# Kernel tuning notes

Hardware: AMD Instinct MI355X
Metric: run time of the kernel (lower is better)

## Reference

```python
import jax, jax.numpy as jnp
import numpy as np
import math

B, T, D = 4, 4096, 512
K_CACHE = 16

def _layernorm(x, g, b, eps=1e-5):
    mu = x.mean(-1, keepdims=True)
    var = ((x - mu) ** 2).mean(-1, keepdims=True)
    return (x - mu) / jnp.sqrt(var + eps) * g + b

def _shift1(x):
    # prepend zero along time axis, drop last: x_prev[t] = x[t-1]
    return jnp.pad(x, ((0, 0), (1, 0), (0, 0)))[:, :-1]

def mipt_parallel_scan(p, theta, inp_re, inp_im):
    # Faithful replication of the torch loop: ceil(log2(T+1)) iterations,
    # each combining with the element shifted by ONE position (as written).
    Bt, Tt, Dt = p.shape
    a_re = (1.0 - p) * jnp.cos(theta)
    a_im = (1.0 - p) * jnp.sin(theta)
    b_re, b_im = inp_re, inp_im
    mask = (jnp.arange(Tt) >= 1)[None, :, None]
    steps = math.ceil(math.log2(Tt + 1))
    for _ in range(steps):
        ar_p, ai_p = _shift1(a_re), _shift1(a_im)
        br_p, bi_p = _shift1(b_re), _shift1(b_im)
        new_a_re = a_re * ar_p - a_im * ai_p
        new_a_im = a_re * ai_p + a_im * ar_p
        new_b_re = a_re * br_p - a_im * bi_p + b_re
        new_b_im = a_re * bi_p + a_im * br_p + b_im
        a_re = jnp.where(mask, new_a_re, a_re)
        a_im = jnp.where(mask, new_a_im, a_im)
        b_re = jnp.where(mask, new_b_re, b_re)
        b_im = jnp.where(mask, new_b_im, b_im)
    return b_re, b_im

def setup_inputs() -> dict:
    key = jax.random.key(0)
    ks = jax.random.split(key, 32)
    s = 0.02
    def W(k, i, o):
        return jax.random.normal(k, (i, o), jnp.float32) * s
    inp = {
        'x': jax.random.normal(ks[0], (B, T, D), jnp.float32),
        'ln1_g': jnp.ones((D,), jnp.float32), 'ln1_b': jnp.zeros((D,), jnp.float32),
        'ln2_g': jnp.ones((D,), jnp.float32), 'ln2_b': jnp.zeros((D,), jnp.float32),
        'Wp_w': W(ks[1], D, D), 'Wp_b': jnp.zeros((D,), jnp.float32),
        'Wt_w': W(ks[2], D, D), 'Wt_b': jnp.zeros((D,), jnp.float32),
        'Wr_w': W(ks[3], D, D), 'Wr_b': jnp.zeros((D,), jnp.float32),
        'Wi_w': W(ks[4], D, D), 'Wi_b': jnp.zeros((D,), jnp.float32),
        'Wk_w': W(ks[5], D, D), 'Wk_b': jnp.zeros((D,), jnp.float32),
        'Wv_w': W(ks[6], D, D), 'Wv_b': jnp.zeros((D,), jnp.float32),
        'Wq_w': W(ks[7], D, D), 'Wq_b': jnp.zeros((D,), jnp.float32),
        'gate_w': W(ks[8], D, 1), 'gate_b': jnp.zeros((1,), jnp.float32),
        'ffn1_w': W(ks[9], D, 4 * D), 'ffn1_b': jnp.zeros((4 * D,), jnp.float32),
        'ffn2_w': W(ks[10], 4 * D, D), 'ffn2_b': jnp.zeros((D,), jnp.float32),
    }
    return inp

def reference(x, ln1_g, ln1_b, ln2_g, ln2_b, Wp_w, Wp_b, Wt_w, Wt_b, Wr_w, Wr_b,
              Wi_w, Wi_b, Wk_w, Wk_b, Wv_w, Wv_b, Wq_w, Wq_b, gate_w, gate_b,
              ffn1_w, ffn1_b, ffn2_w, ffn2_b):
    Bx, Tx, Dx = x.shape
    residual = x
    xn = _layernorm(x, ln1_g, ln1_b)
    p = jax.nn.sigmoid(xn @ Wp_w + Wp_b)
    theta = xn @ Wt_w + Wt_b
    inp_re = xn @ Wr_w + Wr_b
    inp_im = xn @ Wi_w + Wi_b
    h_re, _h_im = mipt_parallel_scan(p, theta, inp_re, inp_im)
    h_mean = h_re.mean(axis=1)  # [B, D]
    # CausalSparseCache (eval mode)
    p_scalar = p.mean(axis=-1)  # [B, T]
    K = min(K_CACHE, Tx)
    _, topk_idx = jax.lax.top_k(p_scalar, K)  # [B, K]
    idx = jnp.broadcast_to(topk_idx[:, :, None], (Bx, K, Dx))
    h_topk = jnp.take_along_axis(h_re, idx, axis=1)  # [B, K, D]
    keys = h_topk @ Wk_w + Wk_b
    values = h_topk @ Wv_w + Wv_b
    query = (h_mean @ Wq_w + Wq_b)[:, None, :]  # [B, 1, D]
    scores = jnp.einsum('bqd,bkd->bqk', query, keys) / math.sqrt(Dx)
    attn = jax.nn.softmax(scores, axis=-1)
    cache_out = jnp.einsum('bqk,bkd->bqd', attn, values)[:, 0]  # [B, D]
    g = jax.nn.sigmoid(h_mean @ gate_w + gate_b)  # [B, 1]
    out = h_mean + g * cache_out
    h = h_re + residual
    hn = _layernorm(h, ln2_g, ln2_b)
    ffn = jax.nn.gelu(hn @ ffn1_w + ffn1_b, approximate=False) @ ffn2_w + ffn2_b
    h = h + ffn
    return (h, out)
```

## Files before the change

kernel.cpp:

```cpp
#include <hip/hip_runtime.h>
#include <hip/hip_bf16.h>
#include <cstdint>
#include <cstddef>

typedef __bf16 bf16;
typedef __attribute__((ext_vector_type(8))) __bf16 bf16x8;
typedef __attribute__((ext_vector_type(4))) __bf16 bf16x4;
typedef __attribute__((ext_vector_type(4))) float f32x4;

#define BB 4
#define TT 4096
#define DD 512
#define MM (BB * TT)
#define OUT1_OFF ((size_t)MM * DD)

typedef __attribute__((address_space(1))) void as1_void;
typedef __attribute__((address_space(3))) void as3_void;

__device__ __forceinline__ void gl_lds16(const void* g, void* l) {
    __builtin_amdgcn_global_load_lds((as1_void*)(uintptr_t)g,
                                     (as3_void*)(uintptr_t)l, 16, 0, 0);
}

#define SIGM(x) (__builtin_amdgcn_rcpf(1.f + __expf(-(x))))

__global__ void transpose_bf16(const float* __restrict__ in, bf16* __restrict__ out,
                               int R, int C) {
    __shared__ float tile[32][33];
    const int c0 = blockIdx.x * 32, r0 = blockIdx.y * 32;
    const int tx = threadIdx.x, ty = threadIdx.y;
#pragma unroll
    for (int i = 0; i < 32; i += 8)
        tile[ty + i][tx] = in[(size_t)(r0 + ty + i) * C + (c0 + tx)];
    __syncthreads();
#pragma unroll
    for (int i = 0; i < 32; i += 8)
        out[(size_t)(c0 + ty + i) * R + (r0 + tx)] = (bf16)tile[tx][ty + i];
}

__global__ void pack_bias(const float* __restrict__ a, const float* __restrict__ b,
                          const float* __restrict__ c, const float* __restrict__ d,
                          float* __restrict__ o) {
    const int i = blockIdx.x * 256 + threadIdx.x;
    if (i < 2048) {
        const float* s = (i < 512) ? a : (i < 1024) ? b : (i < 1536) ? c : d;
        o[i] = s[i & 511];
    }
}

__global__ void zero_kernel(float* __restrict__ p, int n) {
    const int i = blockIdx.x * 256 + threadIdx.x;
    if (i < n) p[i] = 0.f;
}

__global__ __launch_bounds__(256) void ln_kernel(
    const float* __restrict__ X, const bf16* __restrict__ Xadd,
    const float* __restrict__ gw, const float* __restrict__ bw,
    bf16* __restrict__ out) {
    const int row = blockIdx.x * 4 + (threadIdx.x >> 6);
    const int lane = threadIdx.x & 63;
    const float* xr = X + (size_t)row * DD + lane * 8;
    float v[8];
    float4 v0 = *(const float4*)xr;
    float4 v1 = *(const float4*)(xr + 4);
    v[0] = v0.x; v[1] = v0.y; v[2] = v0.z; v[3] = v0.w;
    v[4] = v1.x; v[5] = v1.y; v[6] = v1.z; v[7] = v1.w;
    if (Xadd) {
        const bf16x8 a8 = *(const bf16x8*)(Xadd + (size_t)row * DD + lane * 8);
#pragma unroll
        for (int i = 0; i < 8; ++i) v[i] += (float)a8[i];
    }
    float s = 0.f, ss = 0.f;
#pragma unroll
    for (int i = 0; i < 8; ++i) { s += v[i]; ss += v[i] * v[i]; }
#pragma unroll
    for (int o = 32; o; o >>= 1) { s += __shfl_down(s, o); ss += __shfl_down(ss, o); }
    s = __shfl(s, 0); ss = __shfl(ss, 0);
    const float mu = s * (1.f / DD);
    const float var = ss * (1.f / DD) - mu * mu;
    const float rstd = rsqrtf(var + 1e-5f);
    bf16x8 o8;
#pragma unroll
    for (int i = 0; i < 8; ++i)
        o8[i] = (bf16)((v[i] - mu) * rstd * gw[lane * 8 + i] + bw[lane * 8 + i]);
    *(bf16x8*)(out + (size_t)row * DD + lane * 8) = o8;
}

#define MF(a_, b_, c_) c_ = __builtin_amdgcn_mfma_f32_16x16x32_bf16(a_, b_, c_, 0, 0, 0)

template <int MODE>
__global__ __launch_bounds__(256) void gemm_bt(
    const bf16* __restrict__ A, const bf16* __restrict__ Bt,
    const float* __restrict__ bias, void* __restrict__ Cout,
    void* __restrict__ Cout2,
    const bf16* __restrict__ add1, const float* __restrict__ add2,
    int M, int N, int K) {
    __shared__ bf16 As[3][4096];
    __shared__ bf16 Bs[3][4096];
    const int tid = threadIdx.x;
    const int lane = tid & 63;
    const int wv = tid >> 6;
    const int wr = wv >> 1, wc = wv & 1;
    const int nb = N >> 7;
    const int nwg = gridDim.x;
    int bx = blockIdx.x;
    if ((nwg & 7) == 0) bx = (bx & 7) * (nwg >> 3) + (bx >> 3);
    const int bm = bx / nb, bn = bx % nb;
    const int m0 = bm << 7, n0 = bn << 7;

    const int srow = tid >> 2;
    const int scol = (((tid & 3) ^ ((tid >> 3) & 3)) << 3);
    const bf16* Asrc = A + (size_t)(m0 + srow) * K + scol;
    const bf16* Bsrc = Bt + (size_t)(n0 + srow) * K + scol;
    const size_t rstep = (size_t)64 * K;

    const int lr = lane & 15, lg = lane >> 4;
    const int sel = ((lg ^ ((lr >> 1) & 3)) << 3);
    const int aoff = (wr * 64 + lr) * 32 + sel;
    const int boff = (wc * 64 + lr) * 32 + sel;

#define STG(buf, k0)                                                \
    do {                                                            \
        gl_lds16(Asrc + (k0),         &As[buf][wv * 512]);          \
        gl_lds16(Asrc + (k0) + rstep, &As[buf][wv * 512 + 2048]);   \
        gl_lds16(Bsrc + (k0),         &Bs[buf][wv * 512]);          \
        gl_lds16(Bsrc + (k0) + rstep, &Bs[buf][wv * 512 + 2048]);   \
    } while (0)

    f32x4 acc00 = {}, acc01 = {}, acc02 = {}, acc03 = {};
    f32x4 acc10 = {}, acc11 = {}, acc12 = {}, acc13 = {};
    f32x4 acc20 = {}, acc21 = {}, acc22 = {}, acc23 = {};
    f32x4 acc30 = {}, acc31 = {}, acc32 = {}, acc33 = {};

    const int NT = K >> 5;
    STG(0, 0);
    STG(1, 32);
    int cur = 0;
    for (int t = 0; t < NT; ++t) {
        if (t + 1 < NT) asm volatile("s_waitcnt vmcnt(4)" ::: "memory");
        else            asm volatile("s_waitcnt vmcnt(0)" ::: "memory");
        __builtin_amdgcn_s_barrier();
        asm volatile("" ::: "memory");
        const bf16* Ab = As[cur];
        const bf16* Bb = Bs[cur];
        bf16x8 af0 = *(const bf16x8*)&Ab[aoff];
        bf16x8 af1 = *(const bf16x8*)&Ab[aoff + 512];
        bf16x8 af2 = *(const bf16x8*)&Ab[aoff + 1024];
        bf16x8 af3 = *(const bf16x8*)&Ab[aoff + 1536];
        bf16x8 bf0 = *(const bf16x8*)&Bb[boff];
        bf16x8 bf1 = *(const bf16x8*)&Bb[boff + 512];
        bf16x8 bf2 = *(const bf16x8*)&Bb[boff + 1024];
        bf16x8 bf3 = *(const bf16x8*)&Bb[boff + 1536];
        if (t + 2 < NT) {
            const int stg = (cur == 0) ? 2 : cur - 1;
            STG(stg, (t + 2) << 5);
        }
        MF(af0, bf0, acc00); MF(af0, bf1, acc01); MF(af0, bf2, acc02); MF(af0, bf3, acc03);
        MF(af1, bf0, acc10); MF(af1, bf1, acc11); MF(af1, bf2, acc12); MF(af1, bf3, acc13);
        MF(af2, bf0, acc20); MF(af2, bf1, acc21); MF(af2, bf2, acc22); MF(af2, bf3, acc23);
        MF(af3, bf0, acc30); MF(af3, bf1, acc31); MF(af3, bf2, acc32); MF(af3, bf3, acc33);
        cur = (cur == 2) ? 0 : cur + 1;
    }
#undef STG

    if constexpr (MODE == 0) {
        const int cls = n0 >> 9;
        if (cls == 0) {
            const int pidx = (n0 + wc * 64) >> 6;
#define EPI0(mi, A0, A1, A2, A3)                                              \
    do {                                                                      \
        const int gmb = m0 + wr * 64 + mi * 16 + 4 * lg;                      \
        const int dbase = n0 + wc * 64 + lr;                                  \
        const float b0_ = bias[dbase], b1_ = bias[dbase + 16],                \
                    b2_ = bias[dbase + 32], b3_ = bias[dbase + 48];           \
        _Pragma("unroll")                                                     \
        for (int i = 0; i < 4; ++i) {                                         \
            const int row = gmb + i;                                          \
            const float p0 = SIGM(A0[i] + b0_);                               \
            const float p1 = SIGM(A1[i] + b1_);                               \
            const float p2 = SIGM(A2[i] + b2_);                               \
            const float p3 = SIGM(A3[i] + b3_);                               \
            bf16* ob = (bf16*)Cout + (size_t)row * 2048;                      \
            ob[(size_t)dbase * 4]        = (bf16)(1.f - p0);                  \
            ob[(size_t)(dbase + 16) * 4] = (bf16)(1.f - p1);                  \
            ob[(size_t)(dbase + 32) * 4] = (bf16)(1.f - p2);                  \
            ob[(size_t)(dbase + 48) * 4] = (bf16)(1.f - p3);                  \
            float s_ = p0 + p1 + p2 + p3;                                     \
            s_ += __shfl_xor(s_, 1); s_ += __shfl_xor(s_, 2);                 \
            s_ += __shfl_xor(s_, 4); s_ += __shfl_xor(s_, 8);                 \
            if (lr == 0) ((float*)Cout2)[(size_t)pidx * MM + row] = s_;       \
        }                                                                     \
    } while (0)
            EPI0(0, acc00, acc01, acc02, acc03);
            EPI0(1, acc10, acc11, acc12, acc13);
            EPI0(2, acc20, acc21, acc22, acc23);
            EPI0(3, acc30, acc31, acc32, acc33);
#undef EPI0
        } else {
#define EPIS(mi, ni, ACC)                                                     \
    do {                                                                      \
        const int gmb = m0 + wr * 64 + mi * 16 + 4 * lg;                      \
        const int gn = n0 + wc * 64 + ni * 16 + lr;                           \
        const int dn = gn & 511;                                              \
        const float bia = bias[gn];                                           \
        _Pragma("unroll")                                                     \
        for (int i = 0; i < 4; ++i)                                           \
            ((bf16*)Cout)[((size_t)(gmb + i) * 512 + dn) * 4 + cls] =         \
                (bf16)(ACC[i] + bia);                                         \
    } while (0)
            EPIS(0, 0, acc00); EPIS(0, 1, acc01); EPIS(0, 2, acc02); EPIS(0, 3, acc03);
            EPIS(1, 0, acc10); EPIS(1, 1, acc11); EPIS(1, 2, acc12); EPIS(1, 3, acc13);
            EPIS(2, 0, acc20); EPIS(2, 1, acc21); EPIS(2, 2, acc22); EPIS(2, 3, acc23);
            EPIS(3, 0, acc30); EPIS(3, 1, acc31); EPIS(3, 2, acc32); EPIS(3, 3, acc33);
#undef EPIS
        }
    } else {
#define EPI(mi, ni, ACC)                                                        \
    do {                                                                        \
        const int gmb = m0 + wr * 64 + mi * 16 + 4 * lg;                        \
        const int gn = n0 + wc * 64 + ni * 16 + lr;                             \
        const float bia = bias[gn];                                             \
        _Pragma("unroll")                                                       \
        for (int i = 0; i < 4; ++i) {                                           \
            float v = ACC[i] + bia;                                             \
            const int row = gmb + i;                                            \
            if (MODE == 1) {                                                    \
                const float ge = 0.5f * v * (1.0f + erff(v * 0.70710678118654752f)); \
                ((bf16*)Cout)[(size_t)row * N + gn] = (bf16)ge;                 \
            } else {                                                            \
                const size_t off = (size_t)row * N + gn;                        \
                ((float*)Cout)[off] = v + (float)add1[off] + add2[off];         \
            }                                                                   \
        }                                                                       \
    } while (0)
        EPI(0, 0, acc00); EPI(0, 1, acc01); EPI(0, 2, acc02); EPI(0, 3, acc03);
        EPI(1, 0, acc10); EPI(1, 1, acc11); EPI(1, 2, acc12); EPI(1, 3, acc13);
        EPI(2, 0, acc20); EPI(2, 1, acc21); EPI(2, 2, acc22); EPI(2, 3, acc23);
        EPI(3, 0, acc30); EPI(3, 1, acc31); EPI(3, 2, acc32); EPI(3, 3, acc33);
#undef EPI
    }
}

__global__ __launch_bounds__(256) void pscalar_fin(const float* __restrict__ part,
                                                   float* __restrict__ ps) {
    const int i = blockIdx.x * 256 + threadIdx.x;
    float s = 0.f;
#pragma unroll
    for (int j = 0; j < 8; ++j) s += part[(size_t)j * MM + i];
    ps[i] = s * (1.f / 512.f);
}

#define SCL 32
#define STAGE13(par, pai, pbr, pbi, car, cai, br_, bi_)                     \
    _Pragma("unroll")                                                       \
    for (int k = 0; k < 13; ++k) {                                          \
        const float tar = par[k], tai = pai[k], tbr = pbr[k], tbi = pbi[k]; \
        par[k] = car; pai[k] = cai; pbr[k] = br_; pbi[k] = bi_;             \
        const float nbr = car * tbr - cai * tbi + br_;                      \
        const float nbi = car * tbi + cai * tbr + bi_;                      \
        if (k < 12) {                                                       \
            const float nar = car * tar - cai * tai;                        \
            const float nai = car * tai + cai * tar;                        \
            car = nar; cai = nai;                                           \
        }                                                                   \
        br_ = nbr; bi_ = nbi;                                               \
    }

#define XF(tp, car, cai, br_, bi_)                                       \
    {                                                                    \
        const bf16x4 q_ = *(const bf16x4*)(tp);                          \
        (tp) += 2048;                                                    \
        const float om_ = (float)q_[0];                                  \
        const float th_ = (float)q_[1];                                  \
        br_ = (float)q_[2];                                              \
        bi_ = (float)q_[3];                                              \
        float fr_, sn_, cs_;                                             \
        const float rv_ = th_ * 0.15915494309189535f;                    \
        asm("v_fract_f32 %0, %1" : "=v"(fr_) : "v"(rv_));                \
        asm("v_sin_f32 %0, %1" : "=v"(sn_) : "v"(fr_));                  \
        asm("v_cos_f32 %0, %1" : "=v"(cs_) : "v"(fr_));                  \
        car = om_ * cs_; cai = om_ * sn_;                                \
    }

__global__ __launch_bounds__(256) void scan_kernel(const bf16* __restrict__ lint4,
                                                   bf16* __restrict__ h_re,
                                                   float* __restrict__ hsum) {
    const int blk = blockIdx.x;
    const int b = blk >> 7;
    const int rem = blk & 127;
    const int dh = rem & 1;
    const int tcp = rem >> 1;
    const int d = dh * 256 + threadIdx.x;
    const int t0a = tcp * 64;
    const int t0b = t0a + 32;

    float parA[13], paiA[13], pbrA[13], pbiA[13];
    float parB[13], paiB[13], pbrB[13], pbiB[13];
#pragma unroll
    for (int k = 0; k < 13; ++k) {
        parA[k] = 0.f; paiA[k] = 0.f; pbrA[k] = 0.f; pbiA[k] = 0.f;
        parB[k] = 0.f; paiB[k] = 0.f; pbrB[k] = 0.f; pbiB[k] = 0.f;
    }

    const int warmA = (tcp == 0) ? 0 : 13;
    const bf16* tpA = lint4 + ((size_t)(b * TT + t0a - warmA) * 512 + d) * 4;
    const bf16* tpB = lint4 + ((size_t)(b * TT + t0b - 13) * 512 + d) * 4;
    bf16* poutA = h_re + ((size_t)(b * TT + t0a)) * DD + d;
    bf16* poutB = h_re + ((size_t)(b * TT + t0b)) * DD + d;

    float carA, caiA, brA, biA, carB, caiB, brB, biB;
    for (int s = 0; s < 13; ++s) {
        if (tcp != 0) {
            XF(tpA, carA, caiA, brA, biA)
            STAGE13(parA, paiA, pbrA, pbiA, carA, caiA, brA, biA)
        }
        XF(tpB, carB, caiB, brB, biB)
        STAGE13(parB, paiB, pbrB, pbiB, carB, caiB, brB, biB)
    }

    float hacc = 0.f;
#pragma unroll 2
    for (int s = 0; s < SCL; ++s) {
        XF(tpA, carA, caiA, brA, biA)
        if (tcp == 0 && s == 0) {
#pragma unroll
            for (int k = 0; k < 13; ++k) { parA[k] = carA; paiA[k] = caiA; pbrA[k] = brA; pbiA[k] = biA; }
        } else {
            STAGE13(parA, paiA, pbrA, pbiA, carA, caiA, brA, biA)
        }
        poutA[(size_t)s * DD] = (bf16)brA;
        hacc += brA;
        XF(tpB, carB, caiB, brB, biB)
        STAGE13(parB, paiB, pbrB, pbiB, carB, caiB, brB, biB)
        poutB[(size_t)s * DD] = (bf16)brB;
        hacc += brB;
    }
    atomicAdd(&hsum[b * DD + d], hacc);
}
#undef XF
#undef STAGE13

__global__ __launch_bounds__(256) void topk_kernel(const float* __restrict__ ps,
                                                   int* __restrict__ idx_out) {
    __shared__ float vals[TT];
    __shared__ float rv[4];
    __shared__ int ri[4];
    const int b = blockIdx.x, tid = threadIdx.x;
    for (int i = tid; i < TT; i += 256) vals[i] = ps[b * TT + i];
    __syncthreads();
    for (int kk = 0; kk < 16; ++kk) {
        float bv = -1e30f; int bi = 0x7fffffff;
        for (int i = tid; i < TT; i += 256) {
            const float v = vals[i];
            if (v > bv || (v == bv && i < bi)) { bv = v; bi = i; }
        }
#pragma unroll
        for (int o = 32; o; o >>= 1) {
            const float ov = __shfl_down(bv, o);
            const int oi = __shfl_down(bi, o);
            if (ov > bv || (ov == bv && oi < bi)) { bv = ov; bi = oi; }
        }
        const int lane = tid & 63, wid = tid >> 6;
        if (!lane) { rv[wid] = bv; ri[wid] = bi; }
        __syncthreads();
        if (!tid) {
            float fbv = rv[0]; int fbi = ri[0];
            for (int w = 1; w < 4; ++w)
                if (rv[w] > fbv || (rv[w] == fbv && ri[w] < fbi)) { fbv = rv[w]; fbi = ri[w]; }
            idx_out[b * 16 + kk] = fbi;
            vals[fbi] = -1e30f;
        }
        __syncthreads();
    }
}

__global__ __launch_bounds__(256) void kv_kernel(
    const bf16* __restrict__ h_re, const int* __restrict__ tki,
    const float* __restrict__ Wk, const float* __restrict__ Wkb,
    const float* __restrict__ Wv, const float* __restrict__ Wvb,
    float* __restrict__ keys, float* __restrict__ vals) {
    const int blk = blockIdx.x;
    const int b = blk >> 4, j = blk & 15;
    const int tid = threadIdx.x;
    __shared__ float hrow[512];
    const int row = tki[b * 16 + j];
    for (int i = tid; i < 512; i += 256)
        hrow[i] = (float)h_re[((size_t)(b * TT + row)) * DD + i];
    __syncthreads();
    for (int n = tid; n < 512; n += 256) {
        float sk = Wkb[n], sv = Wvb[n];
        for (int k = 0; k < 512; ++k) {
            const float h = hrow[k];
            sk += h * Wk[(size_t)k * 512 + n];
            sv += h * Wv[(size_t)k * 512 + n];
        }
        keys[((size_t)(b * 16 + j)) * 512 + n] = sk;
        vals[((size_t)(b * 16 + j)) * 512 + n] = sv;
    }
}

__global__ __launch_bounds__(256) void attn_out_kernel(
    const float* __restrict__ hsum, const float* __restrict__ Wq,
    const float* __restrict__ Wqb, const float* __restrict__ gw,
    const float* __restrict__ gb, const float* __restrict__ keys,
    const float* __restrict__ vals, float* __restrict__ out1) {
    const int b = blockIdx.x, tid = threadIdx.x;
    const int lane = tid & 63, wid = tid >> 6;
    __shared__ float hm[512];
    __shared__ float q[512];
    __shared__ float sc[16];
    __shared__ float red[4];
    for (int d0 = tid; d0 < 512; d0 += 256)
        hm[d0] = hsum[b * 512 + d0] * (1.f / 4096.f);
    __syncthreads();
    for (int n = tid; n < 512; n += 256) {
        float s = Wqb[n];
        for (int k = 0; k < 512; ++k) s += hm[k] * Wq[(size_t)k * 512 + n];
        q[n] = s;
    }
    float gp = 0.f;
    for (int k = tid; k < 512; k += 256) gp += hm[k] * gw[k];
#pragma unroll
    for (int o = 32; o; o >>= 1) gp += __shfl_down(gp, o);
    if (!lane) red[wid] = gp;
    __syncthreads();
    const float g = 1.f / (1.f + __expf(-(red[0] + red[1] + red[2] + red[3] + gb[0])));
    for (int kk = wid; kk < 16; kk += 4) {
        float sp = 0.f;
        const float* kr = keys + ((size_t)(b * 16 + kk)) * 512;
        for (int k2 = lane; k2 < 512; k2 += 64) sp += q[k2] * kr[k2];
#pragma unroll
        for (int o = 32; o; o >>= 1) sp += __shfl_down(sp, o);
        if (!lane) sc[kk] = sp * 0.04419417382415922f;
    }
    __syncthreads();
    float mx = sc[0];
#pragma unroll
    for (int kk = 1; kk < 16; ++kk) mx = fmaxf(mx, sc[kk]);
    float den = 0.f;
    float w16[16];
#pragma unroll
    for (int kk = 0; kk < 16; ++kk) { w16[kk] = __expf(sc[kk] - mx); den += w16[kk]; }
    const float rden = 1.f / den;
    for (int d0 = tid; d0 < 512; d0 += 256) {
        float co = 0.f;
#pragma unroll
        for (int kk = 0; kk < 16; ++kk)
            co += w16[kk] * vals[((size_t)(b * 16 + kk)) * 512 + d0];
        out1[b * 512 + d0] = hm[d0] + g * (co * rden);
    }
}

extern "C" void kernel_launch(void* const* d_in, const int* in_sizes, int n_in,
                              void* d_out, int out_size, void* d_ws, size_t ws_size,
                              hipStream_t stream) {
    const float* x    = (const float*)d_in[0];
    const float* ln1g = (const float*)d_in[1];
    const float* ln1b = (const float*)d_in[2];
    const float* ln2g = (const float*)d_in[3];
    const float* ln2b = (const float*)d_in[4];
    const float* Wp_w = (const float*)d_in[5];
    const float* Wp_b = (const float*)d_in[6];
    const float* Wt_w = (const float*)d_in[7];
    const float* Wt_b = (const float*)d_in[8];
    const float* Wr_w = (const float*)d_in[9];
    const float* Wr_b = (const float*)d_in[10];
    const float* Wi_w = (const float*)d_in[11];
    const float* Wi_b = (const float*)d_in[12];
    const float* Wk_w = (const float*)d_in[13];
    const float* Wk_b = (const float*)d_in[14];
    const float* Wv_w = (const float*)d_in[15];
    const float* Wv_b = (const float*)d_in[16];
    const float* Wq_w = (const float*)d_in[17];
    const float* Wq_b = (const float*)d_in[18];
    const float* gw   = (const float*)d_in[19];
    const float* gb   = (const float*)d_in[20];
    const float* f1w  = (const float*)d_in[21];
    const float* f1b  = (const float*)d_in[22];
    const float* f2w  = (const float*)d_in[23];
    const float* f2b  = (const float*)d_in[24];

    char* wsp = (char*)d_ws;
    bf16* lint4 = (bf16*)wsp;
    char* p = wsp + 67108864;
    bf16* h_re = (bf16*)p;   p += 16777216;
    bf16* xn = (bf16*)p;     p += 16777216;
    bf16* hn = (bf16*)p;     p += 16777216;
    bf16* wcat = (bf16*)p;   p += 2097152;
    bf16* f1bt = (bf16*)p;   p += 2097152;
    bf16* f2bt = (bf16*)p;   p += 2097152;
    float* bcat = (float*)p; p += 8192;
    float* ps = (float*)p;   p += 65536;
    float* pspart = (float*)p; p += 524288;
    float* hsum = (float*)p; p += 8192;
    int* tki = (int*)p;      p += 256;
    float* keys = (float*)p; p += 131072;
    float* valsb = (float*)p;
    bf16* act = (bf16*)wsp;
    float* out0 = (float*)d_out;
    float* out1 = (float*)d_out + OUT1_OFF;

    dim3 tb(32, 8);
    transpose_bf16<<<dim3(16, 16), tb, 0, stream>>>(Wp_w, wcat + (size_t)0 * 512 * 512, 512, 512);
    transpose_bf16<<<dim3(16, 16), tb, 0, stream>>>(Wt_w, wcat + (size_t)1 * 512 * 512, 512, 512);
    transpose_bf16<<<dim3(16, 16), tb, 0, stream>>>(Wr_w, wcat + (size_t)2 * 512 * 512, 512, 512);
    transpose_bf16<<<dim3(16, 16), tb, 0, stream>>>(Wi_w, wcat + (size_t)3 * 512 * 512, 512, 512);
    transpose_bf16<<<dim3(64, 16), tb, 0, stream>>>(f1w, f1bt, 512, 2048);
    transpose_bf16<<<dim3(16, 64), tb, 0, stream>>>(f2w, f2bt, 2048, 512);
    pack_bias<<<8, 256, 0, stream>>>(Wp_b, Wt_b, Wr_b, Wi_b, bcat);

    ln_kernel<<<4096, 256, 0, stream>>>(x, nullptr, ln1g, ln1b, xn);
    gemm_bt<0><<<2048, 256, 0, stream>>>(xn, wcat, bcat, lint4, pspart, nullptr, nullptr, MM, 2048, 512);
    pscalar_fin<<<64, 256, 0, stream>>>(pspart, ps);
    zero_kernel<<<8, 256, 0, stream>>>(hsum, 2048);
    scan_kernel<<<512, 256, 0, stream>>>(lint4, h_re, hsum);
    topk_kernel<<<4, 256, 0, stream>>>(ps, tki);
    kv_kernel<<<64, 256, 0, stream>>>(h_re, tki, Wk_w, Wk_b, Wv_w, Wv_b, keys, valsb);
    attn_out_kernel<<<4, 256, 0, stream>>>(hsum, Wq_w, Wq_b, gw, gb, keys, valsb, out1);
    ln_kernel<<<4096, 256, 0, stream>>>(x, h_re, ln2g, ln2b, hn);
    gemm_bt<1><<<2048, 256, 0, stream>>>(hn, f1bt, f1b, act, nullptr, nullptr, nullptr, MM, 2048, 512);
    gemm_bt<2><<<512, 256, 0, stream>>>(act, f2bt, f2b, out0, nullptr, h_re, x, MM, 512, 2048);
}
```

Baseline: 404.8 us.

## Use 256x128 GEMM tiles with 8 waves and a bf16 residual copy of x

The GEMM block tile grows from 128x128 with 4 waves to 256x128 with 8 waves. Each block now stages two A row-halves and one B tile per k-step, so every B tile in LDS is reused across twice as many rows. LN1 also writes a bf16 copy of x, which LN2 and the final residual epilogue read instead of the fp32 input, cutting that read traffic in half. The costs are lower precision in the residual path, more LDS per block, and register pressure under the new launch bounds.

```diff
diff --git a/kernel.cpp b/kernel.cpp
--- a/kernel.cpp
+++ b/kernel.cpp
@@ -53,10 +53,10 @@
     if (i < n) p[i] = 0.f;
 }
 
-__global__ __launch_bounds__(256) void ln_kernel(
-    const float* __restrict__ X, const bf16* __restrict__ Xadd,
-    const float* __restrict__ gw, const float* __restrict__ bw,
-    bf16* __restrict__ out) {
+__global__ __launch_bounds__(256) void ln1_kernel(
+    const float* __restrict__ X, const float* __restrict__ gw,
+    const float* __restrict__ bw, bf16* __restrict__ out,
+    bf16* __restrict__ xbf) {
     const int row = blockIdx.x * 4 + (threadIdx.x >> 6);
     const int lane = threadIdx.x & 63;
     const float* xr = X + (size_t)row * DD + lane * 8;
@@ -65,11 +65,10 @@
     float4 v1 = *(const float4*)(xr + 4);
     v[0] = v0.x; v[1] = v0.y; v[2] = v0.z; v[3] = v0.w;
     v[4] = v1.x; v[5] = v1.y; v[6] = v1.z; v[7] = v1.w;
-    if (Xadd) {
-        const bf16x8 a8 = *(const bf16x8*)(Xadd + (size_t)row * DD + lane * 8);
-#pragma unroll
-        for (int i = 0; i < 8; ++i) v[i] += (float)a8[i];
-    }
+    bf16x8 c8;
+#pragma unroll
+    for (int i = 0; i < 8; ++i) c8[i] = (bf16)v[i];
+    *(bf16x8*)(xbf + (size_t)row * DD + lane * 8) = c8;
     float s = 0.f, ss = 0.f;
 #pragma unroll
     for (int i = 0; i < 8; ++i) { s += v[i]; ss += v[i] * v[i]; }
@@ -86,16 +85,43 @@
     *(bf16x8*)(out + (size_t)row * DD + lane * 8) = o8;
 }
 
+__global__ __launch_bounds__(256) void ln2_kernel(
+    const bf16* __restrict__ Xb, const bf16* __restrict__ Xadd,
+    const float* __restrict__ gw, const float* __restrict__ bw,
+    bf16* __restrict__ out) {
+    const int row = blockIdx.x * 4 + (threadIdx.x >> 6);
+    const int lane = threadIdx.x & 63;
+    const bf16x8 x8 = *(const bf16x8*)(Xb + (size_t)row * DD + lane * 8);
+    const bf16x8 a8 = *(const bf16x8*)(Xadd + (size_t)row * DD + lane * 8);
+    float v[8];
+#pragma unroll
+    for (int i = 0; i < 8; ++i) v[i] = (float)x8[i] + (float)a8[i];
+    float s = 0.f, ss = 0.f;
+#pragma unroll
+    for (int i = 0; i < 8; ++i) { s += v[i]; ss += v[i] * v[i]; }
+#pragma unroll
+    for (int o = 32; o; o >>= 1) { s += __shfl_down(s, o); ss += __shfl_down(ss, o); }
+    s = __shfl(s, 0); ss = __shfl(ss, 0);
+    const float mu = s * (1.f / DD);
+    const float var = ss * (1.f / DD) - mu * mu;
+    const float rstd = rsqrtf(var + 1e-5f);
+    bf16x8 o8;
+#pragma unroll
+    for (int i = 0; i < 8; ++i)
+        o8[i] = (bf16)((v[i] - mu) * rstd * gw[lane * 8 + i] + bw[lane * 8 + i]);
+    *(bf16x8*)(out + (size_t)row * DD + lane * 8) = o8;
+}
+
 #define MF(a_, b_, c_) c_ = __builtin_amdgcn_mfma_f32_16x16x32_bf16(a_, b_, c_, 0, 0, 0)
 
 template <int MODE>
-__global__ __launch_bounds__(256) void gemm_bt(
+__global__ __launch_bounds__(512, 4) void gemm_bt(
     const bf16* __restrict__ A, const bf16* __restrict__ Bt,
     const float* __restrict__ bias, void* __restrict__ Cout,
     void* __restrict__ Cout2,
-    const bf16* __restrict__ add1, const float* __restrict__ add2,
+    const bf16* __restrict__ add1, const bf16* __restrict__ add2,
     int M, int N, int K) {
-    __shared__ bf16 As[3][4096];
+    __shared__ bf16 As[3][8192];
     __shared__ bf16 Bs[3][4096];
     const int tid = threadIdx.x;
     const int lane = tid & 63;
@@ -106,25 +132,24 @@
     int bx = blockIdx.x;
     if ((nwg & 7) == 0) bx = (bx & 7) * (nwg >> 3) + (bx >> 3);
     const int bm = bx / nb, bn = bx % nb;
-    const int m0 = bm << 7, n0 = bn << 7;
+    const int m0 = bm << 8, n0 = bn << 7;
 
     const int srow = tid >> 2;
     const int scol = (((tid & 3) ^ ((tid >> 3) & 3)) << 3);
     const bf16* Asrc = A + (size_t)(m0 + srow) * K + scol;
     const bf16* Bsrc = Bt + (size_t)(n0 + srow) * K + scol;
-    const size_t rstep = (size_t)64 * K;
+    const size_t rstepA = (size_t)128 * K;
 
     const int lr = lane & 15, lg = lane >> 4;
     const int sel = ((lg ^ ((lr >> 1) & 3)) << 3);
     const int aoff = (wr * 64 + lr) * 32 + sel;
     const int boff = (wc * 64 + lr) * 32 + sel;
 
-#define STG(buf, k0)                                                \
-    do {                                                            \
-        gl_lds16(Asrc + (k0),         &As[buf][wv * 512]);          \
-        gl_lds16(Asrc + (k0) + rstep, &As[buf][wv * 512 + 2048]);   \
-        gl_lds16(Bsrc + (k0),         &Bs[buf][wv * 512]);          \
-        gl_lds16(Bsrc + (k0) + rstep, &Bs[buf][wv * 512 + 2048]);   \
+#define STG(buf, k0)                                                 \
+    do {                                                             \
+        gl_lds16(Asrc + (k0),          &As[buf][wv * 512]);          \
+        gl_lds16(Asrc + (k0) + rstepA, &As[buf][wv * 512 + 4096]);   \
+        gl_lds16(Bsrc + (k0),          &Bs[buf][wv * 512]);          \
     } while (0)
 
     f32x4 acc00 = {}, acc01 = {}, acc02 = {}, acc03 = {};
@@ -137,7 +162,7 @@
     STG(1, 32);
     int cur = 0;
     for (int t = 0; t < NT; ++t) {
-        if (t + 1 < NT) asm volatile("s_waitcnt vmcnt(4)" ::: "memory");
+        if (t + 1 < NT) asm volatile("s_waitcnt vmcnt(3)" ::: "memory");
         else            asm volatile("s_waitcnt vmcnt(0)" ::: "memory");
         __builtin_amdgcn_s_barrier();
         asm volatile("" ::: "memory");
@@ -229,7 +254,7 @@
                 ((bf16*)Cout)[(size_t)row * N + gn] = (bf16)ge;                 \
             } else {                                                            \
                 const size_t off = (size_t)row * N + gn;                        \
-                ((float*)Cout)[off] = v + (float)add1[off] + add2[off];         \
+                ((float*)Cout)[off] = v + (float)add1[off] + (float)add2[off];  \
             }                                                                   \
         }                                                                       \
     } while (0)
@@ -486,6 +511,7 @@
     bf16* h_re = (bf16*)p;   p += 16777216;
     bf16* xn = (bf16*)p;     p += 16777216;
     bf16* hn = (bf16*)p;     p += 16777216;
+    bf16* xbf = (bf16*)p;    p += 16777216;
     bf16* wcat = (bf16*)p;   p += 2097152;
     bf16* f1bt = (bf16*)p;   p += 2097152;
     bf16* f2bt = (bf16*)p;   p += 2097152;
@@ -509,15 +535,15 @@
     transpose_bf16<<<dim3(16, 64), tb, 0, stream>>>(f2w, f2bt, 2048, 512);
     pack_bias<<<8, 256, 0, stream>>>(Wp_b, Wt_b, Wr_b, Wi_b, bcat);
 
-    ln_kernel<<<4096, 256, 0, stream>>>(x, nullptr, ln1g, ln1b, xn);
-    gemm_bt<0><<<2048, 256, 0, stream>>>(xn, wcat, bcat, lint4, pspart, nullptr, nullptr, MM, 2048, 512);
+    ln1_kernel<<<4096, 256, 0, stream>>>(x, ln1g, ln1b, xn, xbf);
+    gemm_bt<0><<<1024, 512, 0, stream>>>(xn, wcat, bcat, lint4, pspart, nullptr, nullptr, MM, 2048, 512);
     pscalar_fin<<<64, 256, 0, stream>>>(pspart, ps);
     zero_kernel<<<8, 256, 0, stream>>>(hsum, 2048);
     scan_kernel<<<512, 256, 0, stream>>>(lint4, h_re, hsum);
     topk_kernel<<<4, 256, 0, stream>>>(ps, tki);
     kv_kernel<<<64, 256, 0, stream>>>(h_re, tki, Wk_w, Wk_b, Wv_w, Wv_b, keys, valsb);
     attn_out_kernel<<<4, 256, 0, stream>>>(hsum, Wq_w, Wq_b, gw, gb, keys, valsb, out1);
-    ln_kernel<<<4096, 256, 0, stream>>>(x, h_re, ln2g, ln2b, hn);
-    gemm_bt<1><<<2048, 256, 0, stream>>>(hn, f1bt, f1b, act, nullptr, nullptr, nullptr, MM, 2048, 512);
-    gemm_bt<2><<<512, 256, 0, stream>>>(act, f2bt, f2b, out0, nullptr, h_re, x, MM, 512, 2048);
-}
+    ln2_kernel<<<4096, 256, 0, stream>>>(xbf, h_re, ln2g, ln2b, hn);
+    gemm_bt<1><<<1024, 512, 0, stream>>>(hn, f1bt, f1b, act, nullptr, nullptr, nullptr, MM, 2048, 512);
+    gemm_bt<2><<<256, 512, 0, stream>>>(act, f2bt, f2b, out0, nullptr, h_re, xbf, MM, 512, 2048);
+}
```

Result: faster. 389.9 us (-3.7%).
